# Optimization experiments

Hardware: AMD Instinct MI355X
Metric: run time of the kernel (lower is better)

The kernel has to match this reference:

```python
import jax, jax.numpy as jnp
import numpy as np


def setup_inputs() -> dict:
    key = jax.random.key(0)
    ks = jax.random.split(key, 9)
    B, C, O, T, H, W = 2, 256, 256, 16, 64, 64
    fea_th = jax.random.normal(ks[0], (B, C, T, H), dtype=jnp.float32)
    fea_tw = jax.random.normal(ks[1], (B, C, T, W), dtype=jnp.float32)
    fea_obj = jax.random.normal(ks[2], (B, C, T), dtype=jnp.float32)
    heatmap = jax.random.uniform(ks[3], (B, 1, T, H, W), dtype=jnp.float32)
    mask = jax.random.uniform(ks[4], (B, 1, T, H, W), dtype=jnp.float32)
    s = 1.0 / np.sqrt(C)
    W3d = jax.random.uniform(ks[5], (O, C), dtype=jnp.float32, minval=-s, maxval=s)
    b3d = jax.random.uniform(ks[6], (O,), dtype=jnp.float32, minval=-s, maxval=s)
    W1d = jax.random.uniform(ks[7], (O, C), dtype=jnp.float32, minval=-s, maxval=s)
    b1d = jax.random.uniform(ks[8], (O,), dtype=jnp.float32, minval=-s, maxval=s)
    return {"fea_th": fea_th, "fea_tw": fea_tw, "fea_obj": fea_obj,
            "heatmap": heatmap, "mask": mask,
            "W3d": W3d, "b3d": b3d, "W1d": W1d, "b1d": b1d}


def reference(fea_th, fea_tw, fea_obj, heatmap, mask, W3d, b3d, W1d, b1d):
    # Outer product over spatial dims: [B,C,T,H,1] * [B,C,T,1,W] -> [B,C,T,H,W]
    out_fea = fea_th[..., None] * fea_tw[..., None, :]
    # 1x1x1 Conv3d == channel mixing: bcthw,oc -> bothw (+ bias)
    out_fea = jnp.einsum('bcthw,oc->bothw', out_fea, W3d) + b3d[None, :, None, None, None]
    # 1x1 Conv1d on fea_obj: bct,oc -> bot (+ bias), then broadcast over H,W
    fea_obj_ = (jnp.einsum('bct,oc->bot', fea_obj, W1d) + b1d[None, :, None])[..., None, None]
    # Heatmap blend and mask
    out_fea = out_fea * (1.0 - heatmap) + fea_obj_ * heatmap
    out_fea = out_fea * mask
    return out_fea
```

## Files before the change

kernel.cpp:

```cpp
#include <hip/hip_runtime.h>
#include <hip/hip_bf16.h>

#define B_ 2
#define C_ 256
#define O_ 256
#define T_ 16
#define H_ 64
#define W_ 64

typedef __bf16 bf16x8 __attribute__((ext_vector_type(8)));
typedef float  f32x4  __attribute__((ext_vector_type(4)));

#define WS_OBJ_OFF 131072

__device__ __forceinline__ void gload_lds16(const void* g, void* l) {
    __builtin_amdgcn_global_load_lds(
        (const __attribute__((address_space(1))) void*)g,
        (__attribute__((address_space(3))) void*)l, 16, 0, 0);
}

__global__ __launch_bounds__(256) void prep_kernel(
    const float* __restrict__ fea_obj, const float* __restrict__ W3d,
    const float* __restrict__ W1d, const float* __restrict__ b1d,
    __bf16* __restrict__ wsA, float* __restrict__ wsObj) {
    const int bid = blockIdx.x;
    const int tid = threadIdx.x;
    if (bid < 32) {
        const int b = bid >> 4, t = bid & 15;
        __shared__ float fo[C_];
        fo[tid] = fea_obj[(b * C_ + tid) * T_ + t];
        __syncthreads();
        const int o = tid;
        const float4* wrow = (const float4*)(W1d + o * C_);
        float s = 0.f;
#pragma unroll 8
        for (int cq = 0; cq < C_ / 4; ++cq) {
            float4 wv = wrow[cq];
            s += wv.x * fo[cq * 4 + 0] + wv.y * fo[cq * 4 + 1] +
                 wv.z * fo[cq * 4 + 2] + wv.w * fo[cq * 4 + 3];
        }
        wsObj[(b * T_ + t) * O_ + o] = s + b1d[o];
    } else {
        const int g = (bid - 32) * 256 + tid;
        const int o = g >> 5;
        const int cg = g & 31;
        const float* sp = W3d + o * C_ + cg * 8;
        float4 a0 = *(const float4*)sp;
        float4 a1 = *(const float4*)(sp + 4);
        bf16x8 pk;
        pk[0] = (__bf16)a0.x; pk[1] = (__bf16)a0.y;
        pk[2] = (__bf16)a0.z; pk[3] = (__bf16)a0.w;
        pk[4] = (__bf16)a1.x; pk[5] = (__bf16)a1.y;
        pk[6] = (__bf16)a1.z; pk[7] = (__bf16)a1.w;
        const int mt = o >> 7, o_l = o & 127;
        const int dstb = mt * 65536 + o_l * 512 + ((cg * 16) ^ ((o_l & 7) << 4));
        *(bf16x8*)((char*)wsA + dstb) = pk;
    }
}

__global__ __attribute__((amdgpu_flat_work_group_size(512, 512)))
void main_kernel(
    const float* __restrict__ fea_th, const float* __restrict__ fea_tw,
    const float* __restrict__ heatmap, const float* __restrict__ mask,
    const float* __restrict__ b3d,
    const __bf16* __restrict__ wsA, const float* __restrict__ wsObj,
    float* __restrict__ out) {
    __shared__ __align__(16) char smem[75776];
    char*  sA   = smem;
    float* sTh  = (float*)(smem + 65536);
    float* sPb  = (float*)(smem + 73728);
    float* sObj = (float*)(smem + 74752);

    const int tid  = threadIdx.x;
    const int lane = tid & 63;
    const int wv   = tid >> 6;
    const int wv_m = wv >> 2;
    const int wv_n = wv & 3;
    const int kgrp = lane >> 4;
    const int l15  = lane & 15;

    const int bid = blockIdx.x;
    const int hg = bid & 7, mt = (bid >> 3) & 1, bt = bid >> 4;
    const int b = bt >> 4, t = bt & 15, h0 = hg * 8;

    const char* imgA = (const char*)wsA + mt * 65536;
#pragma unroll
    for (int q = 0; q < 8; ++q)
        gload_lds16(imgA + q * 8192 + tid * 16, sA + q * 8192 + tid * 16);

    const float* objp = wsObj + (b * T_ + t) * O_;
    if (tid < 256) {
        const float* thp = fea_th + ((b * C_ + tid) * T_ + t) * H_ + h0;
        float4 v0 = *(const float4*)thp;
        float4 v1 = *(const float4*)(thp + 4);
        sTh[0 * 256 + tid] = v0.x;  sTh[1 * 256 + tid] = v0.y;
        sTh[2 * 256 + tid] = v0.z;  sTh[3 * 256 + tid] = v0.w;
        sTh[4 * 256 + tid] = v1.x;  sTh[5 * 256 + tid] = v1.y;
        sTh[6 * 256 + tid] = v1.z;  sTh[7 * 256 + tid] = v1.w;
        sPb[tid]  = b3d[tid];
        sObj[tid] = objp[tid];
    }

    const int wcol0 = wv_n * 16 + l15;
    const float* twp = fea_tw + ((b * C_) * T_ + t) * W_;
    bf16x8 twf[8];
#pragma unroll
    for (int ks = 0; ks < 8; ++ks) {
        bf16x8 pk;
#pragma unroll
        for (int j = 0; j < 8; ++j) {
            const int c = ks * 32 + kgrp * 8 + j;
            pk[j] = (__bf16)twp[c * (T_ * W_) + wcol0];
        }
        twf[ks] = pk;
    }

    __syncthreads();

    const int obase = mt * 128 + wv_m * 64 + kgrp * 4;
    const int hmb   = (b * T_ + t) * (H_ * W_);
    const int swz   = (l15 & 7) << 4;
    const int arow  = (wv_m * 64 + l15) * 512;

    for (int hl = 0; hl < 8; ++hl) {
        const int row = hmb + (h0 + hl) * W_ + wcol0;
        const float ht = heatmap[row], mk = mask[row];

        f32x4 acc[4] = {};
#pragma unroll
        for (int ks = 0; ks < 8; ++ks) {
            bf16x8 af[4];
            const int kbyte = (ks * 64 + kgrp * 16) ^ swz;
#pragma unroll
            for (int m = 0; m < 4; ++m)
                af[m] = *(const bf16x8*)(sA + arow + m * 8192 + kbyte);

            const float* thp = sTh + hl * 256 + ks * 32 + kgrp * 8;
            const f32x4 th0 = *(const f32x4*)thp;
            const f32x4 th1 = *(const f32x4*)(thp + 4);

            const bf16x8 tw8 = twf[ks];
            bf16x8 pk;
            pk[0] = (__bf16)((float)tw8[0] * th0[0]);
            pk[1] = (__bf16)((float)tw8[1] * th0[1]);
            pk[2] = (__bf16)((float)tw8[2] * th0[2]);
            pk[3] = (__bf16)((float)tw8[3] * th0[3]);
            pk[4] = (__bf16)((float)tw8[4] * th1[0]);
            pk[5] = (__bf16)((float)tw8[5] * th1[1]);
            pk[6] = (__bf16)((float)tw8[6] * th1[2]);
            pk[7] = (__bf16)((float)tw8[7] * th1[3]);

#pragma unroll
            for (int m = 0; m < 4; ++m)
                acc[m] = __builtin_amdgcn_mfma_f32_16x16x32_bf16(
                    af[m], pk, acc[m], 0, 0, 0);
        }

#pragma unroll
        for (int m = 0; m < 4; ++m) {
            const f32x4 pb4 = *(const f32x4*)(sPb + obase + m * 16);
            const f32x4 po4 = *(const f32x4*)(sObj + obase + m * 16);
#pragma unroll
            for (int r = 0; r < 4; ++r) {
                const int o = obase + m * 16 + r;
                float* orow = out + (((size_t)(b * O_ + o) * T_ + t) * H_ + h0) * W_;
                float v = acc[m][r] + pb4[r];
                v = v * (1.f - ht) + po4[r] * ht;
                orow[hl * W_ + wcol0] = v * mk;
            }
        }
    }
}

extern "C" void kernel_launch(void* const* d_in, const int* in_sizes, int n_in,
                              void* d_out, int out_size, void* d_ws, size_t ws_size,
                              hipStream_t stream) {
    const float* fea_th  = (const float*)d_in[0];
    const float* fea_tw  = (const float*)d_in[1];
    const float* fea_obj = (const float*)d_in[2];
    const float* heatmap = (const float*)d_in[3];
    const float* mask    = (const float*)d_in[4];
    const float* W3d     = (const float*)d_in[5];
    const float* b3d     = (const float*)d_in[6];
    const float* W1d     = (const float*)d_in[7];
    const float* b1d     = (const float*)d_in[8];
    float* out = (float*)d_out;

    __bf16* wsA  = (__bf16*)d_ws;
    float* wsObj = (float*)((char*)d_ws + WS_OBJ_OFF);

    hipLaunchKernelGGL(prep_kernel, dim3(64), dim3(256), 0, stream,
                       fea_obj, W3d, W1d, b1d, wsA, wsObj);
    hipLaunchKernelGGL(main_kernel, dim3(512), dim3(512), 0, stream,
                       fea_th, fea_tw, heatmap, mask, b3d, wsA, wsObj, out);
}
```

Before: 53.94 us.

## Hold W3d fragments in registers and stage outer-product tiles in double-buffered LDS

Each block now covers all 256 output channels for a 32-wide W slice instead of half the channels for the full width. The bf16 weight fragments are loaded straight from global memory into registers, and the fea_th×fea_tw product tile is built into a double-buffered LDS region that is read as the MFMA B operand. This cuts LDS usage and stops re-reading W from LDS on every row. In exchange it adds a __syncthreads per row, uses more registers for weight fragments, and the build step overlaps with the MFMA work.

```diff
diff --git a/kernel.cpp b/kernel.cpp
--- a/kernel.cpp
+++ b/kernel.cpp
@@ -13,16 +13,10 @@
 
 #define WS_OBJ_OFF 131072
 
-__device__ __forceinline__ void gload_lds16(const void* g, void* l) {
-    __builtin_amdgcn_global_load_lds(
-        (const __attribute__((address_space(1))) void*)g,
-        (__attribute__((address_space(3))) void*)l, 16, 0, 0);
-}
-
 __global__ __launch_bounds__(256) void prep_kernel(
     const float* __restrict__ fea_obj, const float* __restrict__ W3d,
     const float* __restrict__ W1d, const float* __restrict__ b1d,
-    __bf16* __restrict__ wsA, float* __restrict__ wsObj) {
+    __bf16* __restrict__ wsW, float* __restrict__ wsObj) {
     const int bid = blockIdx.x;
     const int tid = threadIdx.x;
     if (bid < 32) {
@@ -52,9 +46,7 @@
         pk[2] = (__bf16)a0.z; pk[3] = (__bf16)a0.w;
         pk[4] = (__bf16)a1.x; pk[5] = (__bf16)a1.y;
         pk[6] = (__bf16)a1.z; pk[7] = (__bf16)a1.w;
-        const int mt = o >> 7, o_l = o & 127;
-        const int dstb = mt * 65536 + o_l * 512 + ((cg * 16) ^ ((o_l & 7) << 4));
-        *(bf16x8*)((char*)wsA + dstb) = pk;
+        *(bf16x8*)((char*)wsW + o * 512 + cg * 16) = pk;
     }
 }
 
@@ -63,30 +55,25 @@
     const float* __restrict__ fea_th, const float* __restrict__ fea_tw,
     const float* __restrict__ heatmap, const float* __restrict__ mask,
     const float* __restrict__ b3d,
-    const __bf16* __restrict__ wsA, const float* __restrict__ wsObj,
+    const __bf16* __restrict__ wsW, const float* __restrict__ wsObj,
     float* __restrict__ out) {
-    __shared__ __align__(16) char smem[75776];
-    char*  sA   = smem;
-    float* sTh  = (float*)(smem + 65536);
-    float* sPb  = (float*)(smem + 73728);
-    float* sObj = (float*)(smem + 74752);
+    __shared__ __align__(16) char smem[43008];
+    char*  sB0  = smem;
+    char*  sB1  = smem + 16384;
+    float* sTh  = (float*)(smem + 32768);
+    float* sPb  = (float*)(smem + 40960);
+    float* sObj = (float*)(smem + 41984);
 
     const int tid  = threadIdx.x;
     const int lane = tid & 63;
     const int wv   = tid >> 6;
-    const int wv_m = wv >> 2;
-    const int wv_n = wv & 3;
     const int kgrp = lane >> 4;
     const int l15  = lane & 15;
 
     const int bid = blockIdx.x;
-    const int hg = bid & 7, mt = (bid >> 3) & 1, bt = bid >> 4;
-    const int b = bt >> 4, t = bt & 15, h0 = hg * 8;
-
-    const char* imgA = (const char*)wsA + mt * 65536;
-#pragma unroll
-    for (int q = 0; q < 8; ++q)
-        gload_lds16(imgA + q * 8192 + tid * 16, sA + q * 8192 + tid * 16);
+    const int wb = bid & 1, hg = (bid >> 1) & 7, bt = bid >> 4;
+    const int b = bt >> 4, t = bt & 15;
+    const int h0 = hg * 8, w0 = wb * 32;
 
     const float* objp = wsObj + (b * T_ + t) * O_;
     if (tid < 256) {
@@ -101,74 +88,101 @@
         sObj[tid] = objp[tid];
     }
 
-    const int wcol0 = wv_n * 16 + l15;
-    const float* twp = fea_tw + ((b * C_) * T_ + t) * W_;
-    bf16x8 twf[8];
-#pragma unroll
-    for (int ks = 0; ks < 8; ++ks) {
-        bf16x8 pk;
-#pragma unroll
-        for (int j = 0; j < 8; ++j) {
-            const int c = ks * 32 + kgrp * 8 + j;
-            pk[j] = (__bf16)twp[c * (T_ * W_) + wcol0];
+    const int wl = tid & 31;
+    const int cs = (tid >> 5) * 16;
+    bf16x8 twb0, twb1;
+    {
+        const float* twp = fea_tw + ((b * C_ + cs) * T_ + t) * W_ + w0 + wl;
+#pragma unroll
+        for (int j = 0; j < 8; ++j) twb0[j] = (__bf16)twp[j * (T_ * W_)];
+#pragma unroll
+        for (int j = 0; j < 8; ++j) twb1[j] = (__bf16)twp[(8 + j) * (T_ * W_)];
+    }
+
+    bf16x8 af[2][8];
+#pragma unroll
+    for (int mf = 0; mf < 2; ++mf)
+#pragma unroll
+        for (int ks = 0; ks < 8; ++ks)
+            af[mf][ks] = *(const bf16x8*)(
+                wsW + (wv * 32 + mf * 16 + l15) * 256 + ks * 32 + kgrp * 8);
+
+    const int swzW = (wl & 7) << 4;
+    const int c0g  = (cs >> 3) * 16;
+
+    auto build = [&](int hl, char* dst) {
+        const float* thp = sTh + hl * 256 + cs;
+        const f32x4 t0 = *(const f32x4*)thp;
+        const f32x4 t1 = *(const f32x4*)(thp + 4);
+        const f32x4 t2 = *(const f32x4*)(thp + 8);
+        const f32x4 t3 = *(const f32x4*)(thp + 12);
+        bf16x8 z0, z1;
+        z0[0] = (__bf16)((float)twb0[0] * t0[0]);
+        z0[1] = (__bf16)((float)twb0[1] * t0[1]);
+        z0[2] = (__bf16)((float)twb0[2] * t0[2]);
+        z0[3] = (__bf16)((float)twb0[3] * t0[3]);
+        z0[4] = (__bf16)((float)twb0[4] * t1[0]);
+        z0[5] = (__bf16)((float)twb0[5] * t1[1]);
+        z0[6] = (__bf16)((float)twb0[6] * t1[2]);
+        z0[7] = (__bf16)((float)twb0[7] * t1[3]);
+        z1[0] = (__bf16)((float)twb1[0] * t2[0]);
+        z1[1] = (__bf16)((float)twb1[1] * t2[1]);
+        z1[2] = (__bf16)((float)twb1[2] * t2[2]);
+        z1[3] = (__bf16)((float)twb1[3] * t2[3]);
+        z1[4] = (__bf16)((float)twb1[4] * t3[0]);
+        z1[5] = (__bf16)((float)twb1[5] * t3[1]);
+        z1[6] = (__bf16)((float)twb1[6] * t3[2]);
+        z1[7] = (__bf16)((float)twb1[7] * t3[3]);
+        *(bf16x8*)(dst + wl * 512 + (c0g ^ swzW))        = z0;
+        *(bf16x8*)(dst + wl * 512 + ((c0g + 16) ^ swzW)) = z1;
+    };
+
+    __syncthreads();
+    build(0, sB0);
+    __syncthreads();
+
+    const int hmb  = (b * T_ + t) * (H_ * W_);
+    const int swzR = (l15 & 7) << 4;
+    const int ob0  = wv * 32 + kgrp * 4;
+
+    for (int hl = 0; hl < 8; ++hl) {
+        char* cur = (hl & 1) ? sB1 : sB0;
+        if (hl < 7) build(hl + 1, (hl & 1) ? sB0 : sB1);
+
+        const int hglb = h0 + hl;
+        const int hrow = hmb + hglb * W_ + w0 + l15;
+        const float ht0 = heatmap[hrow],      mk0 = mask[hrow];
+        const float ht1 = heatmap[hrow + 16], mk1 = mask[hrow + 16];
+
+        f32x4 acc[2][2] = {};
+#pragma unroll
+        for (int ks = 0; ks < 8; ++ks) {
+            const int kb = ks * 64 + kgrp * 16;
+            const bf16x8 b0 = *(const bf16x8*)(cur + l15 * 512 + (kb ^ swzR));
+            const bf16x8 b1 = *(const bf16x8*)(cur + (16 + l15) * 512 + (kb ^ swzR));
+            acc[0][0] = __builtin_amdgcn_mfma_f32_16x16x32_bf16(af[0][ks], b0, acc[0][0], 0, 0, 0);
+            acc[0][1] = __builtin_amdgcn_mfma_f32_16x16x32_bf16(af[0][ks], b1, acc[0][1], 0, 0, 0);
+            acc[1][0] = __builtin_amdgcn_mfma_f32_16x16x32_bf16(af[1][ks], b0, acc[1][0], 0, 0, 0);
+            acc[1][1] = __builtin_amdgcn_mfma_f32_16x16x32_bf16(af[1][ks], b1, acc[1][1], 0, 0, 0);
         }
-        twf[ks] = pk;
-    }
-
-    __syncthreads();
-
-    const int obase = mt * 128 + wv_m * 64 + kgrp * 4;
-    const int hmb   = (b * T_ + t) * (H_ * W_);
-    const int swz   = (l15 & 7) << 4;
-    const int arow  = (wv_m * 64 + l15) * 512;
-
-    for (int hl = 0; hl < 8; ++hl) {
-        const int row = hmb + (h0 + hl) * W_ + wcol0;
-        const float ht = heatmap[row], mk = mask[row];
-
-        f32x4 acc[4] = {};
-#pragma unroll
-        for (int ks = 0; ks < 8; ++ks) {
-            bf16x8 af[4];
-            const int kbyte = (ks * 64 + kgrp * 16) ^ swz;
-#pragma unroll
-            for (int m = 0; m < 4; ++m)
-                af[m] = *(const bf16x8*)(sA + arow + m * 8192 + kbyte);
-
-            const float* thp = sTh + hl * 256 + ks * 32 + kgrp * 8;
-            const f32x4 th0 = *(const f32x4*)thp;
-            const f32x4 th1 = *(const f32x4*)(thp + 4);
-
-            const bf16x8 tw8 = twf[ks];
-            bf16x8 pk;
-            pk[0] = (__bf16)((float)tw8[0] * th0[0]);
-            pk[1] = (__bf16)((float)tw8[1] * th0[1]);
-            pk[2] = (__bf16)((float)tw8[2] * th0[2]);
-            pk[3] = (__bf16)((float)tw8[3] * th0[3]);
-            pk[4] = (__bf16)((float)tw8[4] * th1[0]);
-            pk[5] = (__bf16)((float)tw8[5] * th1[1]);
-            pk[6] = (__bf16)((float)tw8[6] * th1[2]);
-            pk[7] = (__bf16)((float)tw8[7] * th1[3]);
-
-#pragma unroll
-            for (int m = 0; m < 4; ++m)
-                acc[m] = __builtin_amdgcn_mfma_f32_16x16x32_bf16(
-                    af[m], pk, acc[m], 0, 0, 0);
-        }
-
-#pragma unroll
-        for (int m = 0; m < 4; ++m) {
-            const f32x4 pb4 = *(const f32x4*)(sPb + obase + m * 16);
-            const f32x4 po4 = *(const f32x4*)(sObj + obase + m * 16);
+
+#pragma unroll
+        for (int mf = 0; mf < 2; ++mf) {
+            const f32x4 pb4 = *(const f32x4*)(sPb + ob0 + mf * 16);
+            const f32x4 po4 = *(const f32x4*)(sObj + ob0 + mf * 16);
 #pragma unroll
             for (int r = 0; r < 4; ++r) {
-                const int o = obase + m * 16 + r;
-                float* orow = out + (((size_t)(b * O_ + o) * T_ + t) * H_ + h0) * W_;
-                float v = acc[m][r] + pb4[r];
-                v = v * (1.f - ht) + po4[r] * ht;
-                orow[hl * W_ + wcol0] = v * mk;
+                const int o = ob0 + mf * 16 + r;
+                float* orow = out + (((size_t)(b * O_ + o) * T_ + t) * H_ + hglb) * W_ + w0;
+                float v0 = acc[mf][0][r] + pb4[r];
+                v0 = v0 * (1.f - ht0) + po4[r] * ht0;
+                orow[l15] = v0 * mk0;
+                float v1 = acc[mf][1][r] + pb4[r];
+                v1 = v1 * (1.f - ht1) + po4[r] * ht1;
+                orow[16 + l15] = v1 * mk1;
             }
         }
+        __syncthreads();
     }
 }
 
@@ -186,11 +200,11 @@
     const float* b1d     = (const float*)d_in[8];
     float* out = (float*)d_out;
 
-    __bf16* wsA  = (__bf16*)d_ws;
+    __bf16* wsW  = (__bf16*)d_ws;
     float* wsObj = (float*)((char*)d_ws + WS_OBJ_OFF);
 
     hipLaunchKernelGGL(prep_kernel, dim3(64), dim3(256), 0, stream,
-                       fea_obj, W3d, W1d, b1d, wsA, wsObj);
+                       fea_obj, W3d, W1d, b1d, wsW, wsObj);
     hipLaunchKernelGGL(main_kernel, dim3(512), dim3(512), 0, stream,
-                       fea_th, fea_tw, heatmap, mask, b3d, wsA, wsObj, out);
+                       fea_th, fea_tw, heatmap, mask, b3d, wsW, wsObj, out);
 }
```

Result: faster. 48.25 us (-10.6%).
